# Optimization experiments

Hardware: AMD Instinct MI355X
Metric: run time of the kernel (lower is better)

The kernel has to match this reference:

```python
import jax, jax.numpy as jnp
import numpy as np


def _pairwise_dist(src, dst):
    # src: [B,K,3,M], dst: [B,K,3,N] -> Euclidean distances [B,K,M,N]
    sq_src = jnp.sum(src * src, axis=2)            # [B,K,M]
    sq_dst = jnp.sum(dst * dst, axis=2)            # [B,K,N]
    cross = jnp.einsum('bkcm,bkcn->bkmn', src, dst)  # [B,K,M,N]
    d2 = sq_src[..., :, None] + sq_dst[..., None, :] - 2.0 * cross
    return jnp.sqrt(jnp.maximum(d2, 0.0))


def setup_inputs() -> dict:
    key = jax.random.key(0)
    k1, k2 = jax.random.split(key)
    B, K, M, N = 16, 8, 1024, 1024
    part_pc_src_input = jax.random.normal(k1, (B, K, 3, M), dtype=jnp.float32)
    part_pc_dst_input = jax.random.normal(k2, (B, K, 3, N), dtype=jnp.float32)
    return {"part_pc_src_input": part_pc_src_input,
            "part_pc_dst_input": part_pc_dst_input}


def reference(part_pc_src_input, part_pc_dst_input):
    # dist[b,k,m,n] = ||src[b,k,:,m] - dst[b,k,:,n]||_2
    dist = _pairwise_dist(part_pc_src_input, part_pc_dst_input)
    # forward: min over dst points, mean over (batch, src points) -> per part [K]
    forward_loss = jnp.min(dist, axis=3).mean(axis=(0, 2))
    # backward: min over src points, mean over (batch, dst points) -> per part [K]
    backward_loss = jnp.min(dist, axis=2).mean(axis=(0, 2))
    chamfer_per_part = forward_loss + backward_loss  # [K]
    return jnp.mean(chamfer_per_part)
```

## Files before the change

kernel.cpp:

```cpp
#include <hip/hip_runtime.h>


typedef float v2f __attribute__((ext_vector_type(2)));

#define NPTS 1024
#define TPB 1024
#define RM 8
#define NCHUNK 4
#define QPC 8

__device__ __forceinline__ v2f pk_fma(v2f a, v2f b, v2f c) {
  v2f d;
  asm("v_pk_fma_f32 %0, %1, %2, %3" : "=v"(d) : "v"(a), "v"(b), "v"(c));
  return d;
}
__device__ __forceinline__ float min3f(float a, float b, float c) {
  float d;
  asm("v_min3_f32 %0, %1, %2, %3" : "=v"(d) : "v"(a), "v"(b), "v"(c));
  return d;
}

__global__ __launch_bounds__(TPB) void chamfer_half_kernel(
    const float* __restrict__ src, const float* __restrict__ dst,
    float* __restrict__ ws,
    int BK) {
  __shared__ float4 rowq[NPTS / 2];
  __shared__ float4 colqA[NPTS / 2];
  __shared__ float4 colqB[NPTS / 2];
  __shared__ unsigned cmb[NPTS];
  __shared__ float wred[16];

  const int t = threadIdx.x;
  const int bk = blockIdx.x >> 1;
  const int half = blockIdx.x & 1;
  const float* S = src + (size_t)bk * 3 * NPTS;
  const float* D = dst + (size_t)bk * 3 * NPTS;

  if (blockIdx.x == 0 && t == 0) ws[0] = 0.0f;

  cmb[t] = 0x7F800000u;
  if (t < NPTS / 2) {
    int m = half * (NPTS / 2) + t;
    float x = S[m], y = S[NPTS + m], z = S[2 * NPTS + m];
    rowq[t] = make_float4(-2.f * x, -2.f * y, -2.f * z,
                          fmaf(x, x, fmaf(y, y, z * z)));
  } else {
    int p = t - NPTS / 2;
    const float2* D2 = (const float2*)D;
    float2 xy = D2[p];
    float2 yy = D2[NPTS / 2 + p];
    float2 zz = D2[NPTS + p];
    colqA[p] = make_float4(xy.x, xy.y, yy.x, yy.y);
    colqB[p] = make_float4(zz.x, zz.y,
                           fmaf(xy.x, xy.x, fmaf(yy.x, yy.x, zz.x * zz.x)),
                           fmaf(xy.y, xy.y, fmaf(yy.y, yy.y, zz.y * zz.y)));
  }
  __syncthreads();

  const int c = t & 15;
  const int r = t >> 4;

  v2f rxp[RM], ryp[RM], rzp[RM], sqp[RM];
  float rmn[RM];
#pragma unroll
  for (int i = 0; i < RM; ++i) {
    float4 q = rowq[r * RM + i];
    rxp[i] = (v2f){q.x, q.x};
    ryp[i] = (v2f){q.y, q.y};
    rzp[i] = (v2f){q.z, q.z};
    sqp[i] = (v2f){q.w, q.w};
    rmn[i] = 3.4e38f;
  }

  for (int k = 0; k < NCHUNK; ++k) {
    v2f cm[QPC];
#pragma unroll
    for (int q = 0; q < QPC; ++q) cm[q] = (v2f){3.4e38f, 3.4e38f};

#pragma unroll
    for (int q = 0; q < QPC; ++q) {
      const int P = k * 128 + q * 16 + c;
      float4 A = colqA[P];
      float4 B = colqB[P];
      v2f xx = {A.x, A.y}, yy = {A.z, A.w};
      v2f zz = {B.x, B.y}, ss = {B.z, B.w};
#pragma unroll
      for (int i = 0; i < RM; i += 2) {
        v2f v0 = pk_fma(rzp[i], zz, ss);
        v2f v1 = pk_fma(rzp[i + 1], zz, ss);
        v0 = pk_fma(ryp[i], yy, v0);
        v1 = pk_fma(ryp[i + 1], yy, v1);
        v0 = pk_fma(rxp[i], xx, v0);
        v1 = pk_fma(rxp[i + 1], xx, v1);
        rmn[i] = min3f(rmn[i], v0.x, v0.y);
        rmn[i + 1] = min3f(rmn[i + 1], v1.x, v1.y);
        v2f cv0 = v0 + sqp[i];
        v2f cv1 = v1 + sqp[i + 1];
        cm[q].x = min3f(cm[q].x, cv0.x, cv1.x);
        cm[q].y = min3f(cm[q].y, cv0.y, cv1.y);
      }
    }
#pragma unroll
    for (int q = 0; q < QPC; ++q) {
      float a = cm[q].x, b = cm[q].y;
      a = fminf(a, __shfl_xor(a, 16)); a = fminf(a, __shfl_xor(a, 32));
      b = fminf(b, __shfl_xor(b, 16)); b = fminf(b, __shfl_xor(b, 32));
      if (((t >> 4) & 3) == 0) {
        const int P = k * 128 + q * 16 + c;
        atomicMin(&cmb[2 * P], __float_as_uint(fmaxf(a, 0.f)));
        atomicMin(&cmb[2 * P + 1], __float_as_uint(fmaxf(b, 0.f)));
      }
    }
  }

  float rsum = 0.f;
#pragma unroll
  for (int i = 0; i < RM; ++i) {
    float a = rmn[i];
    a = fminf(a, __shfl_xor(a, 1));
    a = fminf(a, __shfl_xor(a, 2));
    a = fminf(a, __shfl_xor(a, 4));
    a = fminf(a, __shfl_xor(a, 8));
    rsum += sqrtf(fmaxf(sqp[i].x + a, 0.f));
  }
  float v = (c == 0) ? rsum : 0.f;
  for (int off = 32; off; off >>= 1) v += __shfl_down(v, off);
  if ((t & 63) == 0) wred[t >> 6] = v;
  __syncthreads();

  if (t == 0) {
    float s = 0.f;
#pragma unroll
    for (int w = 0; w < 16; ++w) s += wred[w];
    ws[64 + blockIdx.x] = s;
  }
  float* colpart = ws + 1024;
  colpart[((size_t)half * BK + bk) * NPTS + t] = __uint_as_float(cmb[t]);
}

__global__ __launch_bounds__(256) void chamfer_merge_kernel(
    const float* __restrict__ ws, float* __restrict__ acc, int BK) {
  const int bk = blockIdx.x;
  const int t = threadIdx.x;
  const float* colpart = ws + 1024;
  const float4* c0 = (const float4*)(colpart + (size_t)bk * NPTS);
  const float4* c1 = (const float4*)(colpart + ((size_t)BK + bk) * NPTS);
  float4 a = c0[t], b = c1[t];
  float s = sqrtf(fminf(a.x, b.x)) + sqrtf(fminf(a.y, b.y)) +
            sqrtf(fminf(a.z, b.z)) + sqrtf(fminf(a.w, b.w));
  if (t < 2) s += ws[64 + 2 * bk + t];
  for (int off = 32; off; off >>= 1) s += __shfl_down(s, off);
  __shared__ float wr[4];
  if ((t & 63) == 0) wr[t >> 6] = s;
  __syncthreads();
  if (t == 0) atomicAdd(acc, wr[0] + wr[1] + wr[2] + wr[3]);
}

__global__ void chamfer_scale_kernel(const float* __restrict__ acc,
                                     float* __restrict__ out, float scale) {
  if (threadIdx.x == 0) out[0] = acc[0] * scale;
}

extern "C" void kernel_launch(void* const* d_in, const int* in_sizes, int n_in,
                              void* d_out, int out_size, void* d_ws, size_t ws_size,
                              hipStream_t stream) {
  const float* src = (const float*)d_in[0];
  const float* dst = (const float*)d_in[1];
  float* out = (float*)d_out;
  float* ws = (float*)d_ws;

  const int BK = in_sizes[0] / (3 * NPTS);
  const float scale = 1.0f / (float)(BK * NPTS);

  chamfer_half_kernel<<<dim3(2 * BK), TPB, 0, stream>>>(src, dst, ws, BK);
  chamfer_merge_kernel<<<dim3(BK), 256, 0, stream>>>(ws, ws, BK);
  chamfer_scale_kernel<<<dim3(1), 64, 0, stream>>>(ws, out, scale);
}
```

Baseline: 82.35 us.

## Compute pairwise squared distances with bf16 split-precision MFMA and runtime layout probe

```diff
diff --git a/kernel.cpp b/kernel.cpp
--- a/kernel.cpp
+++ b/kernel.cpp
@@ -1,133 +1,240 @@
 #include <hip/hip_runtime.h>
 
 
-typedef float v2f __attribute__((ext_vector_type(2)));
+typedef __attribute__((ext_vector_type(8))) short bf16x8;
+typedef __attribute__((ext_vector_type(4))) float f32x4;
 
 #define NPTS 1024
 #define TPB 1024
-#define RM 8
-#define NCHUNK 4
-#define QPC 8
-
-__device__ __forceinline__ v2f pk_fma(v2f a, v2f b, v2f c) {
-  v2f d;
-  asm("v_pk_fma_f32 %0, %1, %2, %3" : "=v"(d) : "v"(a), "v"(b), "v"(c));
-  return d;
-}
-__device__ __forceinline__ float min3f(float a, float b, float c) {
-  float d;
-  asm("v_min3_f32 %0, %1, %2, %3" : "=v"(d) : "v"(a), "v"(b), "v"(c));
-  return d;
-}
-
-__global__ __launch_bounds__(TPB) void chamfer_half_kernel(
+
+__device__ __forceinline__ ushort bf16h(float f) {
+  unsigned b = __float_as_uint(f);
+  return (ushort)((b + 0x7FFFu + ((b >> 16) & 1u)) >> 16);
+}
+__device__ __forceinline__ float bf16f(ushort h) {
+  return __uint_as_float((unsigned)h << 16);
+}
+__device__ __forceinline__ f32x4 MFMA(bf16x8 a, bf16x8 b, f32x4 c) {
+  return __builtin_amdgcn_mfma_f32_16x16x32_bf16(a, b, c, 0, 0, 0);
+}
+__device__ __forceinline__ float d2ref_(const float* P, const float* Q,
+                                        int i, int j) {
+  float dx = P[i] - Q[j];
+  float dy = P[NPTS + i] - Q[NPTS + j];
+  float dz = P[2 * NPTS + i] - Q[2 * NPTS + j];
+  return fmaf(dx, dx, fmaf(dy, dy, dz * dz));
+}
+
+__global__ __launch_bounds__(TPB) void chamfer_k1(
     const float* __restrict__ src, const float* __restrict__ dst,
-    float* __restrict__ ws,
-    int BK) {
-  __shared__ float4 rowq[NPTS / 2];
-  __shared__ float4 colqA[NPTS / 2];
-  __shared__ float4 colqB[NPTS / 2];
+    float* __restrict__ ws, int BK) {
+  __shared__ uint4 fragA[512 * 2];
+  __shared__ uint4 fragB[1024 * 2];
   __shared__ unsigned cmb[NPTS];
   __shared__ float wred[16];
+  __shared__ float4 rowF[512];
+  __shared__ float4 colF[1024];
+  __shared__ int s_mode;
 
   const int t = threadIdx.x;
-  const int bk = blockIdx.x >> 1;
-  const int half = blockIdx.x & 1;
+  const int lane = t & 63;
+  const int m16 = lane & 15;
+  const int kb = lane >> 4;
+  const int wv = t >> 6;
+  const int bk = blockIdx.x >> 1, half = blockIdx.x & 1;
   const float* S = src + (size_t)bk * 3 * NPTS;
   const float* D = dst + (size_t)bk * 3 * NPTS;
 
-  if (blockIdx.x == 0 && t == 0) ws[0] = 0.0f;
-
+  if (blockIdx.x == 0 && t == 0) ws[0] = 0.f;
   cmb[t] = 0x7F800000u;
-  if (t < NPTS / 2) {
-    int m = half * (NPTS / 2) + t;
+
+  const unsigned ONE = 0x3F80u;
+  if (t < 512) {
+    const int m = half * 512 + t;
     float x = S[m], y = S[NPTS + m], z = S[2 * NPTS + m];
-    rowq[t] = make_float4(-2.f * x, -2.f * y, -2.f * z,
-                          fmaf(x, x, fmaf(y, y, z * z)));
+    float sq = fmaf(x, x, fmaf(y, y, z * z));
+    float ux = -2.f * x, uy = -2.f * y, uz = -2.f * z;
+    unsigned xh = bf16h(ux), yh = bf16h(uy), zh = bf16h(uz);
+    unsigned xl = bf16h(ux - bf16f(xh)), yl = bf16h(uy - bf16f(yh)),
+             zl = bf16h(uz - bf16f(zh));
+    unsigned sh = bf16h(sq), sl = bf16h(sq - bf16f(sh));
+    fragA[t * 2] = make_uint4(xh | (yh << 16), zh | (xh << 16),
+                              yh | (zh << 16), xl | (yl << 16));
+    fragA[t * 2 + 1] = make_uint4(zl | (sh << 16), sl | (ONE << 16), ONE, 0u);
+  }
+  {
+    float x = D[t], y = D[NPTS + t], z = D[2 * NPTS + t];
+    float sq = fmaf(x, x, fmaf(y, y, z * z));
+    unsigned xh = bf16h(x), yh = bf16h(y), zh = bf16h(z);
+    unsigned xl = bf16h(x - bf16f(xh)), yl = bf16h(y - bf16f(yh)),
+             zl = bf16h(z - bf16f(zh));
+    unsigned sh = bf16h(sq), sl = bf16h(sq - bf16f(sh));
+    fragB[t * 2] = make_uint4(xh | (yh << 16), zh | (xl << 16),
+                              yl | (zl << 16), xh | (yh << 16));
+    fragB[t * 2 + 1] = make_uint4(zh | (ONE << 16), ONE | (sh << 16), sl, 0u);
+  }
+  __syncthreads();
+
+  const f32x4 cz = {0.f, 0.f, 0.f, 0.f};
+  bf16x8 z8;
+#pragma unroll
+  for (int j = 0; j < 8; ++j) z8[j] = 0;
+  bf16x8 pa = z8, pb = z8;
+#pragma unroll
+  for (int j = 0; j < 8; ++j) pa[j] = (short)bf16h((float)(kb * 8 + j));
+  f32x4 q0 = MFMA(pa, pa, cz);
+  int ok0 = (q0[0] == 10416.f) && (q0[1] == 10416.f) &&
+            (q0[2] == 10416.f) && (q0[3] == 10416.f);
+  pa = z8; pb = z8;
+  if (kb == 0) { pa[0] = (short)bf16h(1.f); pb[0] = (short)bf16h((float)(1 + m16)); }
+  f32x4 q1 = MFMA(pa, pb, cz);
+  pa = z8; pb = z8;
+  if (kb == 0) { pa[0] = (short)bf16h((float)(1 + m16)); pb[0] = (short)bf16h(1.f); }
+  f32x4 q2 = MFMA(pa, pb, cz);
+
+  int colm = 1, rowm = 1, gokv = 1;
+  int gofs[4];
+#pragma unroll
+  for (int r = 0; r < 4; ++r) {
+    colm &= (q1[r] == (float)(1 + m16));
+    rowm &= (q2[r] == (float)(1 + m16));
+    gofs[r] = (int)q1[r] - 1;
+    gokv &= (gofs[r] >= 0 && gofs[r] < 16);
+  }
+  colm = __all(colm && ok0);
+  rowm = __all(rowm && ok0);
+  gokv = __all(gokv);
+
+  if (wv == 0) {
+    int mode = (colm && !rowm) ? 0 : ((rowm && !colm && gokv) ? 1 : 2);
+    if (mode != 2) {
+      bf16x8 a0 = *(const bf16x8*)&fragA[(m16 * 2) + (kb & 1)];
+      if (kb >= 2) a0 = z8;
+      bf16x8 b0 = *(const bf16x8*)&fragB[(m16 * 2) + (kb & 1)];
+      f32x4 dchk = MFMA(a0, b0, cz);
+      float s4 = dchk[0] + dchk[1] + dchk[2] + dchk[3];
+      float refg = 0.f, refr = 0.f;
+#pragma unroll
+      for (int r = 0; r < 4; ++r) {
+        int ig = 4 * kb + r, ir = kb + 4 * r;
+        refg += d2ref_(S, D, half * 512 + (mode == 0 ? ig : m16),
+                       (mode == 0 ? m16 : ig));
+        refr += d2ref_(S, D, half * 512 + (mode == 0 ? ir : m16),
+                       (mode == 0 ? m16 : ir));
+      }
+      int cg = fabsf(s4 - refg) <= 0.1f + 5e-3f * fabsf(refg);
+      int cr = fabsf(s4 - refr) <= 0.1f + 5e-3f * fabsf(refr);
+      if (!__all(cg) && !__all(cr)) mode = 2;
+    }
+    if (lane == 0) s_mode = mode;
+  }
+  __syncthreads();
+  const int mode = s_mode;
+
+  float rs = 0.f;
+
+  if (mode == 0 || mode == 1) {
+    bf16x8 a0 = *(const bf16x8*)&fragA[(((wv * 2 + 0) * 16 + m16) * 2) + (kb & 1)];
+    bf16x8 a1 = *(const bf16x8*)&fragA[(((wv * 2 + 1) * 16 + m16) * 2) + (kb & 1)];
+    if (kb >= 2) { a0 = z8; a1 = z8; }
+    float r0[4], r1[4];
+#pragma unroll
+    for (int r = 0; r < 4; ++r) { r0[r] = 3.4e38f; r1[r] = 3.4e38f; }
+
+    if (mode == 0) {
+      for (int ct = 0; ct < 64; ++ct) {
+        bf16x8 b = *(const bf16x8*)&fragB[((ct * 16 + m16) * 2) + (kb & 1)];
+        f32x4 d0 = MFMA(a0, b, cz);
+        f32x4 d1 = MFMA(a1, b, cz);
+#pragma unroll
+        for (int r = 0; r < 4; ++r) {
+          r0[r] = fminf(r0[r], d0[r]);
+          r1[r] = fminf(r1[r], d1[r]);
+        }
+        float c = fminf(fminf(d0[0], d0[1]), fminf(d0[2], d0[3]));
+        c = fminf(c, fminf(fminf(d1[0], d1[1]), fminf(d1[2], d1[3])));
+        c = fminf(c, __shfl_xor(c, 16));
+        c = fminf(c, __shfl_xor(c, 32));
+        if (kb == 0)
+          atomicMin(&cmb[ct * 16 + m16], __float_as_uint(fmaxf(c, 0.f)));
+      }
+#pragma unroll
+      for (int r = 0; r < 4; ++r) {
+        float v = r0[r];
+        v = fminf(v, __shfl_xor(v, 1));
+        v = fminf(v, __shfl_xor(v, 2));
+        v = fminf(v, __shfl_xor(v, 4));
+        v = fminf(v, __shfl_xor(v, 8));
+        rs += sqrtf(fmaxf(v, 0.f));
+        v = r1[r];
+        v = fminf(v, __shfl_xor(v, 1));
+        v = fminf(v, __shfl_xor(v, 2));
+        v = fminf(v, __shfl_xor(v, 4));
+        v = fminf(v, __shfl_xor(v, 8));
+        rs += sqrtf(fmaxf(v, 0.f));
+      }
+      rs = (m16 == 0) ? rs : 0.f;
+    } else {
+      for (int ct = 0; ct < 64; ++ct) {
+        bf16x8 b = *(const bf16x8*)&fragB[((ct * 16 + m16) * 2) + (kb & 1)];
+        f32x4 d0 = MFMA(a0, b, cz);
+        f32x4 d1 = MFMA(a1, b, cz);
+#pragma unroll
+        for (int r = 0; r < 4; ++r) {
+          r0[r] = fminf(r0[r], d0[r]);
+          r1[r] = fminf(r1[r], d1[r]);
+          float c = fminf(d0[r], d1[r]);
+          c = fminf(c, __shfl_xor(c, 1));
+          c = fminf(c, __shfl_xor(c, 2));
+          c = fminf(c, __shfl_xor(c, 4));
+          c = fminf(c, __shfl_xor(c, 8));
+          if (m16 == 0)
+            atomicMin(&cmb[ct * 16 + gofs[r]], __float_as_uint(fmaxf(c, 0.f)));
+        }
+      }
+      float vA = fminf(fminf(r0[0], r0[1]), fminf(r0[2], r0[3]));
+      vA = fminf(vA, __shfl_xor(vA, 16));
+      vA = fminf(vA, __shfl_xor(vA, 32));
+      float vB = fminf(fminf(r1[0], r1[1]), fminf(r1[2], r1[3]));
+      vB = fminf(vB, __shfl_xor(vB, 16));
+      vB = fminf(vB, __shfl_xor(vB, 32));
+      rs = sqrtf(fmaxf(vA, 0.f)) + sqrtf(fmaxf(vB, 0.f));
+      rs = (kb == 0) ? rs : 0.f;
+    }
   } else {
-    int p = t - NPTS / 2;
-    const float2* D2 = (const float2*)D;
-    float2 xy = D2[p];
-    float2 yy = D2[NPTS / 2 + p];
-    float2 zz = D2[NPTS + p];
-    colqA[p] = make_float4(xy.x, xy.y, yy.x, yy.y);
-    colqB[p] = make_float4(zz.x, zz.y,
-                           fmaf(xy.x, xy.x, fmaf(yy.x, yy.x, zz.x * zz.x)),
-                           fmaf(xy.y, xy.y, fmaf(yy.y, yy.y, zz.y * zz.y)));
-  }
-  __syncthreads();
-
-  const int c = t & 15;
-  const int r = t >> 4;
-
-  v2f rxp[RM], ryp[RM], rzp[RM], sqp[RM];
-  float rmn[RM];
-#pragma unroll
-  for (int i = 0; i < RM; ++i) {
-    float4 q = rowq[r * RM + i];
-    rxp[i] = (v2f){q.x, q.x};
-    ryp[i] = (v2f){q.y, q.y};
-    rzp[i] = (v2f){q.z, q.z};
-    sqp[i] = (v2f){q.w, q.w};
-    rmn[i] = 3.4e38f;
-  }
-
-  for (int k = 0; k < NCHUNK; ++k) {
-    v2f cm[QPC];
-#pragma unroll
-    for (int q = 0; q < QPC; ++q) cm[q] = (v2f){3.4e38f, 3.4e38f};
-
-#pragma unroll
-    for (int q = 0; q < QPC; ++q) {
-      const int P = k * 128 + q * 16 + c;
-      float4 A = colqA[P];
-      float4 B = colqB[P];
-      v2f xx = {A.x, A.y}, yy = {A.z, A.w};
-      v2f zz = {B.x, B.y}, ss = {B.z, B.w};
-#pragma unroll
-      for (int i = 0; i < RM; i += 2) {
-        v2f v0 = pk_fma(rzp[i], zz, ss);
-        v2f v1 = pk_fma(rzp[i + 1], zz, ss);
-        v0 = pk_fma(ryp[i], yy, v0);
-        v1 = pk_fma(ryp[i + 1], yy, v1);
-        v0 = pk_fma(rxp[i], xx, v0);
-        v1 = pk_fma(rxp[i + 1], xx, v1);
-        rmn[i] = min3f(rmn[i], v0.x, v0.y);
-        rmn[i + 1] = min3f(rmn[i + 1], v1.x, v1.y);
-        v2f cv0 = v0 + sqp[i];
-        v2f cv1 = v1 + sqp[i + 1];
-        cm[q].x = min3f(cm[q].x, cv0.x, cv1.x);
-        cm[q].y = min3f(cm[q].y, cv0.y, cv1.y);
-      }
-    }
-#pragma unroll
-    for (int q = 0; q < QPC; ++q) {
-      float a = cm[q].x, b = cm[q].y;
-      a = fminf(a, __shfl_xor(a, 16)); a = fminf(a, __shfl_xor(a, 32));
-      b = fminf(b, __shfl_xor(b, 16)); b = fminf(b, __shfl_xor(b, 32));
-      if (((t >> 4) & 3) == 0) {
-        const int P = k * 128 + q * 16 + c;
-        atomicMin(&cmb[2 * P], __float_as_uint(fmaxf(a, 0.f)));
-        atomicMin(&cmb[2 * P + 1], __float_as_uint(fmaxf(b, 0.f)));
-      }
-    }
-  }
-
-  float rsum = 0.f;
-#pragma unroll
-  for (int i = 0; i < RM; ++i) {
-    float a = rmn[i];
-    a = fminf(a, __shfl_xor(a, 1));
-    a = fminf(a, __shfl_xor(a, 2));
-    a = fminf(a, __shfl_xor(a, 4));
-    a = fminf(a, __shfl_xor(a, 8));
-    rsum += sqrtf(fmaxf(sqp[i].x + a, 0.f));
-  }
-  float v = (c == 0) ? rsum : 0.f;
+    if (t < 512) {
+      int m = half * 512 + t;
+      rowF[t] = make_float4(S[m], S[NPTS + m], S[2 * NPTS + m], 0.f);
+    }
+    colF[t] = make_float4(D[t], D[NPTS + t], D[2 * NPTS + t], 0.f);
+    __syncthreads();
+    if (t < 512) {
+      float4 p = rowF[t];
+      float mn = 3.4e38f;
+      for (int n = 0; n < NPTS; ++n) {
+        float4 q = colF[n];
+        float dx = p.x - q.x, dy = p.y - q.y, dz = p.z - q.z;
+        mn = fminf(mn, fmaf(dx, dx, fmaf(dy, dy, dz * dz)));
+      }
+      rs = sqrtf(mn);
+    }
+    {
+      float4 q = colF[t];
+      float mc = 3.4e38f;
+      for (int m = 0; m < 512; ++m) {
+        float4 p = rowF[m];
+        float dx = p.x - q.x, dy = p.y - q.y, dz = p.z - q.z;
+        mc = fminf(mc, fmaf(dx, dx, fmaf(dy, dy, dz * dz)));
+      }
+      cmb[t] = __float_as_uint(mc);
+    }
+  }
+
+  __syncthreads();
+  float v = rs;
   for (int off = 32; off; off >>= 1) v += __shfl_down(v, off);
-  if ((t & 63) == 0) wred[t >> 6] = v;
-  __syncthreads();
-
+  if (lane == 0) wred[wv] = v;
+  __syncthreads();
   if (t == 0) {
     float s = 0.f;
 #pragma unroll
@@ -172,7 +279,7 @@
   const int BK = in_sizes[0] / (3 * NPTS);
   const float scale = 1.0f / (float)(BK * NPTS);
 
-  chamfer_half_kernel<<<dim3(2 * BK), TPB, 0, stream>>>(src, dst, ws, BK);
+  chamfer_k1<<<dim3(2 * BK), TPB, 0, stream>>>(src, dst, ws, BK);
   chamfer_merge_kernel<<<dim3(BK), 256, 0, stream>>>(ws, ws, BK);
   chamfer_scale_kernel<<<dim3(1), 64, 0, stream>>>(ws, out, scale);
 }
```

New measurement: 81.50 us. Within noise of the previous version (-1.0%).
